# Optimization experiments

Measured on AMD Instinct MI355X. Metric: run time of the kernel, lower is better.

The kernel has to match this reference:

```python
import math
import jax, jax.numpy as jnp
import numpy as np

N_HEADS = 16

def _alibi_slopes(n_heads: int) -> np.ndarray:
    def pow2_slopes(n):
        start = 2 ** (-2 ** (-(math.log2(n) - 3)))
        return [start * start ** i for i in range(n)]
    if math.log2(n_heads).is_integer():
        slopes = pow2_slopes(n_heads)
    else:
        closest = 2 ** math.floor(math.log2(n_heads))
        slopes = pow2_slopes(closest)
        extra = pow2_slopes(2 * closest)[0::2]
        slopes = slopes + extra[: n_heads - closest]
    return np.asarray(slopes, dtype=np.float32)

def _build_alibi_bias(n_heads: int, T: int) -> jnp.ndarray:
    # (1, H, T, T): lower triangle = -slope*|i-j|, strict upper = -inf (causal)
    slopes = jnp.asarray(_alibi_slopes(n_heads))  # (H,)
    pos = jnp.arange(T)
    dist = pos[None, :] - pos[None, :].T  # (T, T), j - i
    causal = dist < 0  # future positions (j > i means dist>0? note: dist = j - i transposed)
    # match torch: distances = positions[None,:] - positions[:,None] -> dist[i,j] = j - i
    dist = pos[None, :] - pos[:, None]
    causal = dist > 0  # wait: torch masks distances < 0 where distances[i,j] = j - i? No:
    # torch: distances = positions.unsqueeze(0) - positions.unsqueeze(1) -> dist[i,j] = positions[j] - positions[i]? 
    # unsqueeze(0): (1,T) row j; unsqueeze(1): (T,1) row i -> dist[i,j] = pos[j] - pos[i]
    # causal_mask = dist < 0 masks j < i ... but then bias upper triangle kept?
    # Actually torch masks where distances < 0, i.e., j < i (past). That seems inverted,
    # but we must be FAITHFUL: mask fills -inf where pos[j] - pos[i] < 0.
    d = pos[None, :] - pos[:, None]  # d[i,j] = j - i
    mask = d < 0
    bias = -slopes[:, None, None] * jnp.abs(d).astype(jnp.float32)[None, :, :]
    bias = jnp.where(mask[None, :, :], -jnp.inf, bias)
    return bias[None]  # (1, H, T, T)

def setup_inputs() -> dict:
    key = jax.random.key(0)
    k1, k2, k3 = jax.random.split(key, 3)
    B, T, D = 2, 2048, 1024
    x = jax.random.normal(k1, (B, T, D), dtype=jnp.float32)
    W_qkv = jax.random.normal(k2, (D, 3 * D), dtype=jnp.float32) * (1.0 / math.sqrt(D))
    W_out = jax.random.normal(k3, (D, D), dtype=jnp.float32) * (1.0 / math.sqrt(D))
    return {"x": x, "W_qkv": W_qkv, "W_out": W_out}

def reference(x, W_qkv, W_out):
    B, T, D = x.shape
    H = N_HEADS
    hd = D // H
    qkv = x @ W_qkv  # (B, T, 3D)
    q, k, v = jnp.split(qkv, 3, axis=-1)
    q = q.reshape(B, T, H, hd).transpose(0, 2, 1, 3)  # (B,H,T,hd)
    k = k.reshape(B, T, H, hd).transpose(0, 2, 1, 3)
    v = v.reshape(B, T, H, hd).transpose(0, 2, 1, 3)
    scale = 1.0 / math.sqrt(hd)
    attn = jnp.einsum('bhqd,bhkd->bhqk', q, k) * scale  # (B,H,T,T)
    attn = attn + _build_alibi_bias(H, T)
    attn = jax.nn.softmax(attn, axis=-1)
    out = jnp.einsum('bhqk,bhkd->bhqd', attn, v)  # (B,H,T,hd)
    out = out.transpose(0, 2, 1, 3).reshape(B, T, D)
    return out @ W_out
```

## Files before the change

### kernel.cpp

```cpp
#include <hip/hip_runtime.h>

#define DEV __device__ __forceinline__

typedef __attribute__((ext_vector_type(4))) float f32x4;
typedef __attribute__((ext_vector_type(16))) float f32x16;
typedef __attribute__((ext_vector_type(8))) short s16x8;

static constexpr int TB  = 2;
static constexpr int TT  = 2048;
static constexpr int TD  = 1024;
static constexpr int TH  = 16;
static constexpr int THD = 64;
static constexpr int TN3 = 3072;
static constexpr int TM  = TB * TT;

#define WS_FLAG   0u
#define WS_XB     1024u
#define WS_WQKVT  (WS_XB + 8388608u)
#define WS_WOUTT  (WS_WQKVT + 6291456u)
#define WS_QKV    (WS_WOUTT + 2097152u)
#define WS_VT     (WS_QKV + 25165824u)
#define WS_CTX    (WS_VT + 8388608u)

DEV unsigned short f2bf(float f) {
  unsigned int u = __builtin_bit_cast(unsigned int, f);
  u += 0x7FFFu + ((u >> 16) & 1u);
  return (unsigned short)(u >> 16);
}
DEV f32x4 mfma16(s16x8 a, s16x8 b, f32x4 c) {
  return __builtin_amdgcn_mfma_f32_16x16x32_bf16(a, b, c, 0, 0, 0);
}
DEV f32x16 mfma32(s16x8 a, s16x8 b, f32x16 c) {
  return __builtin_amdgcn_mfma_f32_32x32x16_bf16(a, b, c, 0, 0, 0);
}
DEV void gload_lds16(const void* g, void* l) {
  __builtin_amdgcn_global_load_lds(
      (const __attribute__((address_space(1))) void*)g,
      (__attribute__((address_space(3))) void*)l, 16, 0, 0);
}
DEV unsigned int cvtpk(float lo, float hi_) {
  unsigned int r;
  asm("v_cvt_pk_bf16_f32 %0, %1, %2" : "=v"(r) : "v"(lo), "v"(hi_));
  return r;
}
DEV void plswap(unsigned int& a, unsigned int& b) {
  asm("v_permlane32_swap_b32 %0, %1" : "+v"(a), "+v"(b));
}

__global__ __launch_bounds__(256) void detect_kernel(const uint4* __restrict__ probe,
                                                     int* __restrict__ flag) {
  __shared__ int cnt;
  if (threadIdx.x == 0) cnt = 0;
  __syncthreads();
  uint4 v = probe[threadIdx.x];
  int local = 0;
  unsigned int w[4] = {v.x, v.y, v.z, v.w};
#pragma unroll
  for (int k = 0; k < 4; ++k) {
    unsigned int e0 = (w[k] >> 7) & 0xFF;
    unsigned int e1 = (w[k] >> 23) & 0xFF;
    if (e0 >= 135) local++;
    if (e1 >= 135) local++;
  }
  atomicAdd(&cnt, local);
  __syncthreads();
  if (threadIdx.x == 0) flag[0] = (cnt < 100) ? 1 : 0;
}

__global__ __launch_bounds__(256) void prep_kernel(const void* __restrict__ x,
                                                   const void* __restrict__ wqkv,
                                                   const void* __restrict__ wout,
                                                   unsigned short* __restrict__ xb,
                                                   unsigned short* __restrict__ wqkvt,
                                                   unsigned short* __restrict__ woutt,
                                                   const int* __restrict__ flag) {
  __shared__ unsigned short tile[64 * 65];
  const int bid = blockIdx.x;
  const bool bf = (flag[0] != 0);
  if (bid < 1024) {
    const void* W; unsigned short* Wt; int N, k0, n0;
    if (bid < 768) { W = wqkv; Wt = wqkvt; N = TN3; k0 = (bid & 15) * 64; n0 = (bid >> 4) * 64; }
    else { int id = bid - 768; W = wout; Wt = woutt; N = TD; k0 = (id & 15) * 64; n0 = (id >> 4) * 64; }
    for (int e = threadIdx.x; e < 4096; e += 256) {
      int kr = e >> 6, nc = e & 63;
      unsigned short v;
      if (bf) v = ((const unsigned short*)W)[(size_t)(k0 + kr) * N + n0 + nc];
      else    v = f2bf(((const float*)W)[(size_t)(k0 + kr) * N + n0 + nc]);
      tile[kr * 65 + nc] = v;
    }
    __syncthreads();
    for (int e = threadIdx.x; e < 4096; e += 256) {
      int nr = e >> 6, kc = e & 63;
      Wt[(size_t)(n0 + nr) * TD + k0 + kc] = tile[kc * 65 + nr];
    }
  } else {
    int i = (bid - 1024) * 256 + threadIdx.x;
    if (i >= (TM * TD) / 8) return;
    if (bf) {
      ((uint4*)xb)[i] = ((const uint4*)x)[i];
    } else {
      const float* s = (const float*)x + (size_t)i * 8;
      unsigned int w0 = (unsigned int)f2bf(s[0]) | ((unsigned int)f2bf(s[1]) << 16);
      unsigned int w1 = (unsigned int)f2bf(s[2]) | ((unsigned int)f2bf(s[3]) << 16);
      unsigned int w2 = (unsigned int)f2bf(s[4]) | ((unsigned int)f2bf(s[5]) << 16);
      unsigned int w3 = (unsigned int)f2bf(s[6]) | ((unsigned int)f2bf(s[7]) << 16);
      uint4 o; o.x = w0; o.y = w1; o.z = w2; o.w = w3;
      ((uint4*)xb)[i] = o;
    }
  }
}

__global__ __launch_bounds__(512, 2) void gemm_8p_kernel(const unsigned short* __restrict__ A,
                                                         const unsigned short* __restrict__ Bt,
                                                         unsigned short* __restrict__ C,
                                                         unsigned short* __restrict__ vtb,
                                                         int Mn, int Nn, int Kn) {
  __shared__ unsigned short lA[2][256 * 64];
  __shared__ unsigned short lB[2][256 * 64];
  const int tid = threadIdx.x;
  const int lane = tid & 63;
  const int wid = tid >> 6;
  const int wm = wid >> 2, wn = wid & 3;
  const int l15 = lane & 15, lg = lane >> 4;

  const int nby = Nn >> 8;
  const int nwg = (Mn >> 8) * nby;
  const int cpx = nwg >> 3;
  const int bid = blockIdx.x;
  const int swz = (bid & 7) * cpx + (bid >> 3);
  const int bm = swz / nby, bn = swz % nby;
  const int row0 = bm << 8, col0 = bn << 8;

  const int srow = tid >> 3;
  const int scol = ((tid & 7) ^ (srow & 7)) * 8;
  const unsigned short* aS = A  + (size_t)(row0 + srow) * Kn + scol;
  const unsigned short* bS = Bt + (size_t)(col0 + srow) * Kn + scol;
  const size_t r64 = (size_t)64 * Kn;

#define STG(dst, src, koff, h) do {                                        \
    unsigned short* _d = (dst) + (h) * 8192 + tid * 8;                     \
    const unsigned short* _s = (src) + (size_t)(h) * 2 * r64 + (koff);     \
    gload_lds16(_s, _d);                                                   \
    gload_lds16(_s + r64, _d + 4096);                                      \
  } while (0)

  f32x4 acc[8][4];
#pragma unroll
  for (int m = 0; m < 8; ++m)
#pragma unroll
    for (int n = 0; n < 4; ++n) acc[m][n] = (f32x4){0.f, 0.f, 0.f, 0.f};

  const int sa = l15 & 7;
  const int kc0 = (lg ^ sa) * 8;
  const int kc1 = ((4 + lg) ^ sa) * 8;
  const int aRow = (wm * 128 + l15) * 64;
  const int bRow = (wn * 64 + l15) * 64;

  STG(&lA[0][0], aS, 0, 0); STG(&lA[0][0], aS, 0, 1);
  STG(&lB[0][0], bS, 0, 0); STG(&lB[0][0], bS, 0, 1);
  asm volatile("s_waitcnt vmcnt(0)" ::: "memory");
  __builtin_amdgcn_s_barrier();

  const int nt = Kn >> 6;
  for (int t = 0; t < nt; ++t) {
    const unsigned short* la = &lA[t & 1][0];
    const unsigned short* lb = &lB[t & 1][0];
    unsigned short* na = &lA[(t + 1) & 1][0];
    unsigned short* nb = &lB[(t + 1) & 1][0];
    const int koff = (t + 1) << 6;
    const bool more = (t + 1 < nt);

    s16x8 af[4][2], b0[2][2], b1[2][2];

#pragma unroll
    for (int m = 0; m < 4; ++m) {
      af[m][0] = *(const s16x8*)&la[aRow + m * 1024 + kc0];
      af[m][1] = *(const s16x8*)&la[aRow + m * 1024 + kc1];
    }
#pragma unroll
    for (int n = 0; n < 2; ++n) {
      b0[n][0] = *(const s16x8*)&lb[bRow + n * 1024 + kc0];
      b0[n][1] = *(const s16x8*)&lb[bRow + n * 1024 + kc1];
    }
    if (more) STG(na, aS, koff, 0);
    __builtin_amdgcn_s_barrier();
    asm volatile("s_waitcnt lgkmcnt(0)" ::: "memory");
    __builtin_amdgcn_sched_barrier(0);
    __builtin_amdgcn_s_setprio(1);
#pragma unroll
    for (int m = 0; m < 4; ++m)
#pragma unroll
      for (int n = 0; n < 2; ++n) {
        acc[m][n] = mfma16(af[m][0], b0[n][0], acc[m][n]);
        acc[m][n] = mfma16(af[m][1], b0[n][1], acc[m][n]);
      }
    __builtin_amdgcn_s_setprio(0);
    if (more) asm volatile("s_waitcnt vmcnt(4)" ::: "memory");
    else      asm volatile("s_waitcnt vmcnt(1)" ::: "memory");
    __builtin_amdgcn_s_barrier();

#pragma unroll
    for (int n = 0; n < 2; ++n) {
      b1[n][0] = *(const s16x8*)&lb[bRow + (2 + n) * 1024 + kc0];
      b1[n][1] = *(const s16x8*)&lb[bRow + (2 + n) * 1024 + kc1];
    }
    if (more) STG(nb, bS, koff, 0);
    __builtin_amdgcn_s_barrier();
    asm volatile("s_waitcnt lgkmcnt(0)" ::: "memory");
    __builtin_amdgcn_sched_barrier(0);
    __builtin_amdgcn_s_setprio(1);
#pragma unroll
    for (int m = 0; m < 4; ++m)
#pragma unroll
      for (int n = 0; n < 2; ++n) {
        acc[m][2 + n] = mfma16(af[m][0], b1[n][0], acc[m][2 + n]);
        acc[m][2 + n] = mfma16(af[m][1], b1[n][1], acc[m][2 + n]);
      }
    __builtin_amdgcn_s_setprio(0);
    if (more) asm volatile("s_waitcnt vmcnt(4)" ::: "memory");
    else      asm volatile("s_waitcnt vmcnt(0)" ::: "memory");
    __builtin_amdgcn_s_barrier();

#pragma unroll
    for (int m = 0; m < 4; ++m) {
      af[m][0] = *(const s16x8*)&la[aRow + (4 + m) * 1024 + kc0];
      af[m][1] = *(const s16x8*)&la[aRow + (4 + m) * 1024 + kc1];
    }
    if (more) STG(nb, bS, koff, 1);
    __builtin_amdgcn_s_barrier();
    asm volatile("s_waitcnt lgkmcnt(0)" ::: "memory");
    __builtin_amdgcn_sched_barrier(0);
    __builtin_amdgcn_s_setprio(1);
#pragma unroll
    for (int m = 0; m < 4; ++m)
#pragma unroll
      for (int n = 0; n < 2; ++n) {
        acc[4 + m][n] = mfma16(af[m][0], b0[n][0], acc[4 + m][n]);
        acc[4 + m][n] = mfma16(af[m][1], b0[n][1], acc[4 + m][n]);
      }
    __builtin_amdgcn_s_setprio(0);
    __builtin_amdgcn_s_barrier();

    if (more) STG(na, aS, koff, 1);
    __builtin_amdgcn_s_barrier();
    __builtin_amdgcn_sched_barrier(0);
    __builtin_amdgcn_s_setprio(1);
#pragma unroll
    for (int m = 0; m < 4; ++m)
#pragma unroll
      for (int n = 0; n < 2; ++n) {
        acc[4 + m][2 + n] = mfma16(af[m][0], b1[n][0], acc[4 + m][2 + n]);
        acc[4 + m][2 + n] = mfma16(af[m][1], b1[n][1], acc[4 + m][2 + n]);
      }
    __builtin_amdgcn_s_setprio(0);
    if (more) asm volatile("s_waitcnt vmcnt(4)" ::: "memory");
    __builtin_amdgcn_s_barrier();
  }
#undef STG

  if (col0 < 2048) {
    unsigned short* cw = C + (size_t)(row0 + wm * 128 + lg * 4) * Nn + col0 + wn * 64 + l15;
#pragma unroll
    for (int m = 0; m < 8; ++m)
#pragma unroll
      for (int n = 0; n < 4; ++n)
#pragma unroll
        for (int j = 0; j < 4; ++j)
          cw[(size_t)(m * 16 + j) * Nn + n * 16] = f2bf(acc[m][n][j]);
  } else {
    const int cb0 = col0 + wn * 64 + l15 - 2048;
    const int t0r = row0 + wm * 128 + lg * 4;
#pragma unroll
    for (int m = 0; m < 8; ++m) {
      int tg = t0r + m * 16;
      int bb = tg >> 11, tt = tg & 2047;
#pragma unroll
      for (int n = 0; n < 4; ++n) {
        int cc2 = cb0 + n * 16;
        int h = cc2 >> 6, d = cc2 & 63;
        unsigned short* dst = vtb + (((size_t)(bb * 16 + h) * 64 + d) << 11) + tt;
        uint2 pk;
        pk.x = cvtpk(acc[m][n][0], acc[m][n][1]);
        pk.y = cvtpk(acc[m][n][2], acc[m][n][3]);
        *(uint2*)dst = pk;
      }
    }
  }
}

__global__ __launch_bounds__(256) void gemm_bt2_kernel(const unsigned short* __restrict__ A,
                                                       const unsigned short* __restrict__ Bt,
                                                       void* __restrict__ Cout,
                                                       int Mn, int Nn, int Kn,
                                                       const int* __restrict__ flag) {
  __shared__ unsigned short lA[2][128 * 32];
  __shared__ unsigned short lB[2][64 * 32];
  const int tid  = threadIdx.x;
  const int lane = tid & 63, wid = tid >> 6;
  const int wr = wid >> 1, wc = wid & 1;
  const int l15 = lane & 15, lg = lane >> 4;
  const int row0 = blockIdx.x * 128, col0 = blockIdx.y * 64;

  f32x4 acc[4][2];
#pragma unroll
  for (int m = 0; m < 4; ++m)
#pragma unroll
    for (int n = 0; n < 2; ++n) acc[m][n] = (f32x4){0.f, 0.f, 0.f, 0.f};

  const int srow = tid >> 2;
  const int scol = ((tid & 3) ^ (srow & 3)) * 8;
  const unsigned short* aS = A  + (size_t)(row0 + srow) * Kn + scol;
  const unsigned short* bS = Bt + (size_t)(col0 + srow) * Kn + scol;
  const size_t r64 = (size_t)64 * Kn;

#define STG2(bi) do {                                        \
    unsigned short* _da = &lA[bi][0] + tid * 8;              \
    gload_lds16(aS,       _da);                              \
    gload_lds16(aS + r64, _da + 2048);                       \
    if (srow < 64) gload_lds16(bS, &lB[bi][0] + tid * 8);    \
  } while (0)

  const int rd = (lg ^ (l15 & 3)) * 8;
  const int aoff = (wr * 64 + l15) * 32 + rd;
  const int boff = (wc * 32 + l15) * 32 + rd;

  STG2(0); aS += 32; bS += 32;
  __syncthreads();

  const int nt = Kn >> 5;
  for (int t = 0; t < nt; ++t) {
    if (t + 1 < nt) { STG2((t + 1) & 1); aS += 32; bS += 32; }
    const unsigned short* la = &lA[t & 1][0];
    const unsigned short* lb = &lB[t & 1][0];
    s16x8 af[4], bfv[2];
#pragma unroll
    for (int m = 0; m < 4; ++m) af[m] = *(const s16x8*)&la[aoff + m * 512];
#pragma unroll
    for (int n = 0; n < 2; ++n) bfv[n] = *(const s16x8*)&lb[boff + n * 512];
    __builtin_amdgcn_s_setprio(1);
#pragma unroll
    for (int m = 0; m < 4; ++m)
#pragma unroll
      for (int n = 0; n < 2; ++n)
        acc[m][n] = mfma16(af[m], bfv[n], acc[m][n]);
    __builtin_amdgcn_s_setprio(0);
    __syncthreads();
  }
#undef STG2

  const bool obf = (flag[0] != 0);
#pragma unroll
  for (int m = 0; m < 4; ++m)
#pragma unroll
    for (int n = 0; n < 2; ++n)
#pragma unroll
      for (int j = 0; j < 4; ++j) {
        int r = row0 + wr * 64 + m * 16 + lg * 4 + j;
        int c = col0 + wc * 32 + n * 16 + l15;
        if (obf) ((unsigned short*)Cout)[(size_t)r * Nn + c] = f2bf(acc[m][n][j]);
        else     ((float*)Cout)[(size_t)r * Nn + c] = acc[m][n][j];
      }
}

__global__ __launch_bounds__(256, 4) void attn_kernel(const unsigned short* __restrict__ qkv,
                                                      const unsigned short* __restrict__ vt,
                                                      unsigned short* __restrict__ ctx) {
  __shared__ __align__(16) unsigned char smem[32768];
  unsigned short* kl0 = (unsigned short*)smem;
  unsigned short* vl0 = (unsigned short*)(smem + 16384);
  float* red = (float*)smem;

  const int bid = blockIdx.x;
  const int r_ = bid & 255, q_ = bid >> 8;
  const int s_ = r_ >> 5, g_ = r_ & 31;
  const int bh = (g_ + 8 * q_) & 31;
  const int x32 = (q_ == 0) ? s_ : (q_ == 1) ? 15 - s_ : (q_ == 2) ? 16 + s_ : 31 - s_;
  const int b = bh >> 4, h = bh & 15;

  const int tid = threadIdx.x;
  const int wid = tid >> 6, lane = tid & 63;
  const int wr = wid & 1, wk = wid >> 1;
  const int l31 = lane & 31, hi = lane >> 5;
  const int i_base = x32 * 64 + wr * 32;

  const unsigned short* qb  = qkv + (size_t)b * TT * TN3 + h * THD;
  const unsigned short* kb_ = qkv + (size_t)b * TT * TN3 + TD + h * THD;
  const unsigned short* vb_ = vt + (size_t)bh * THD * TT;

  const float LOG2E = 1.44269504f;
  const float SL2 = exp2f(-0.5f * (float)(h + 1)) * LOG2E;
  const float SC2 = 0.125f * LOG2E;
  const float dbias = -SL2 * 64.0f;

  const int t_rel = (int)((140.0f / SL2 + 63.0f) * (1.0f / 64.0f)) + 1;
  const int t_end = (32 < x32 + t_rel) ? 32 : x32 + t_rel;

  const int srow = tid >> 3;
  const int sx = ((tid & 7) ^ (srow & 7)) * 8;
  const unsigned short* srcK = kb_ + (size_t)(x32 * 64 + srow) * TN3 + sx;
  const unsigned short* srcV = vb_ + (size_t)srow * TT + x32 * 64 + sx;
  const size_t kstep = (size_t)64 * TN3;

#define STAGE(bufi) do {                                   \
    unsigned short* _dk = kl0 + (bufi) * 4096 + tid * 8;   \
    unsigned short* _dv = vl0 + (bufi) * 4096 + tid * 8;   \
    gload_lds16(srcK,            _dk);                     \
    gload_lds16(srcK + 32 * TN3, _dk + 2048);              \
    gload_lds16(srcV,            _dv);                     \
    gload_lds16(srcV + 32 * TT,  _dv + 2048);              \
  } while (0)

  s16x8 qa[4];
  {
    const unsigned short* qr = qb + (size_t)(i_base + l31) * TN3 + hi * 8;
#pragma unroll
    for (int dd = 0; dd < 4; ++dd) qa[dd] = *(const s16x8*)(qr + dd * 16);
  }

  s16x8 ones;
  {
    short ov = (l31 == 0) ? (short)0x3F80 : (short)0;
#pragma unroll
    for (int e = 0; e < 8; ++e) ones[e] = ov;
  }

  float base[16];
#pragma unroll
  for (int r = 0; r < 16; ++r) {
    int cr0 = (r & 3) + 8 * (r >> 2);
    base[r] = -SL2 * (float)(wk * 32 + cr0 + 4 * hi - wr * 32 - l31) - 16.0f;
  }

  f32x16 o0, o1, ol;
#pragma unroll
  for (int r = 0; r < 16; ++r) { o0[r] = 0.f; o1[r] = 0.f; ol[r] = 0.f; }

  const int sw = (l31 & 7) << 4;
  int cc[4];
#pragma unroll
  for (int dd = 0; dd < 4; ++dd) cc[dd] = ((dd * 32 + hi * 16) ^ sw) >> 1;

  int cur = 0;
  STAGE(0); srcK += kstep; srcV += 64;
  asm volatile("s_waitcnt vmcnt(0)" ::: "memory");
  __syncthreads();

  for (int t = x32; t < t_end; ++t) {
    if (t + 1 < t_end) { STAGE(cur ^ 1); srcK += kstep; srcV += 64; }

    const unsigned short* kb = kl0 + cur * 4096;
    const unsigned short* vbl = vl0 + cur * 4096;

    f32x16 sv;
#pragma unroll
    for (int r = 0; r < 16; ++r) sv[r] = 0.f;
    __builtin_amdgcn_s_setprio(1);
#pragma unroll
    for (int dd = 0; dd < 4; ++dd) {
      s16x8 k0 = *(const s16x8*)&kb[(wk * 32 + l31) * 64 + cc[dd]];
      sv = mfma32(k0, qa[dd], sv);
    }
    __builtin_amdgcn_s_setprio(0);

    if (t == x32) {
#pragma unroll
      for (int r = 0; r < 16; ++r) {
        float bb = base[r];
        float v = __builtin_amdgcn_exp2f(fmaf(sv[r], SC2, bb));
        sv[r] = (bb > -15.999f) ? 0.0f : v;
      }
    } else {
#pragma unroll
      for (int r = 0; r < 16; ++r)
        sv[r] = __builtin_amdgcn_exp2f(fmaf(sv[r], SC2, base[r]));
    }
#pragma unroll
    for (int r = 0; r < 16; ++r) base[r] += dbias;

    s16x8 pa[2];
#pragma unroll
    for (int mh = 0; mh < 2; ++mh) {
      unsigned int a0 = cvtpk(sv[8 * mh + 0], sv[8 * mh + 1]);
      unsigned int a1 = cvtpk(sv[8 * mh + 2], sv[8 * mh + 3]);
      unsigned int b0 = cvtpk(sv[8 * mh + 4], sv[8 * mh + 5]);
      unsigned int b1 = cvtpk(sv[8 * mh + 6], sv[8 * mh + 7]);
      plswap(a0, b0); plswap(a1, b1);
      uint4 u; u.x = a0; u.y = a1; u.z = b0; u.w = b1;
      pa[mh] = __builtin_bit_cast(s16x8, u);
    }

    __builtin_amdgcn_s_setprio(1);
#pragma unroll
    for (int ks = 0; ks < 2; ++ks) {
      s16x8 v0 = *(const s16x8*)&vbl[l31 * 64 + cc[wk * 2 + ks]];
      s16x8 v1 = *(const s16x8*)&vbl[(32 + l31) * 64 + cc[wk * 2 + ks]];
      o0 = mfma32(pa[ks], v0, o0);
      o1 = mfma32(pa[ks], v1, o1);
      ol = mfma32(pa[ks], ones, ol);
    }
    __builtin_amdgcn_s_setprio(0);

    asm volatile("s_waitcnt vmcnt(0)" ::: "memory");
    __syncthreads();
    cur ^= 1;
  }
#undef STAGE

  const int rbase = (wr * 64 + lane) * 49;
  if (wk == 1) {
#pragma unroll
    for (int r = 0; r < 16; ++r) red[rbase + r] = o0[r];
#pragma unroll
    for (int r = 0; r < 16; ++r) red[rbase + 16 + r] = o1[r];
#pragma unroll
    for (int r = 0; r < 16; ++r) red[rbase + 32 + r] = ol[r];
  }
  __syncthreads();
  if (wk == 0) {
#pragma unroll
    for (int r = 0; r < 16; ++r) o0[r] += red[rbase + r];
#pragma unroll
    for (int r = 0; r < 16; ++r) o1[r] += red[rbase + 16 + r];
#pragma unroll
    for (int r = 0; r < 16; ++r) ol[r] += red[rbase + 32 + r];

    float rdiv[16];
#pragma unroll
    for (int r = 0; r < 16; ++r) rdiv[r] = 1.0f / __shfl(ol[r], lane & 32);

    unsigned short* cb = ctx + (size_t)(b * TT + i_base) * TD + h * THD + l31;
#pragma unroll
    for (int r = 0; r < 16; ++r) {
      int row = (r & 3) + 8 * (r >> 2) + 4 * hi;
      unsigned int pk = cvtpk(o0[r] * rdiv[r], o1[r] * rdiv[r]);
      cb[(size_t)row * TD] = (unsigned short)pk;
      cb[(size_t)row * TD + 32] = (unsigned short)(pk >> 16);
    }
  }
}

extern "C" void kernel_launch(void* const* d_in, const int* in_sizes, int n_in,
                              void* d_out, int out_size, void* d_ws, size_t ws_size,
                              hipStream_t stream) {
  const void* x    = d_in[0];
  const void* wqkv = d_in[1];
  const void* wout = d_in[2];
  char* ws = (char*)d_ws;
  int* flag             = (int*)(ws + WS_FLAG);
  unsigned short* xb    = (unsigned short*)(ws + WS_XB);
  unsigned short* wqkvt = (unsigned short*)(ws + WS_WQKVT);
  unsigned short* woutt = (unsigned short*)(ws + WS_WOUTT);
  unsigned short* qkvb  = (unsigned short*)(ws + WS_QKV);
  unsigned short* vtb   = (unsigned short*)(ws + WS_VT);
  unsigned short* ctxb  = (unsigned short*)(ws + WS_CTX);

  detect_kernel<<<1, 256, 0, stream>>>((const uint4*)x, flag);
  prep_kernel<<<3072, 256, 0, stream>>>(x, wqkv, wout, xb, wqkvt, woutt, flag);
  gemm_8p_kernel<<<(TM / 256) * (TN3 / 256), 512, 0, stream>>>(xb, wqkvt, qkvb, vtb, TM, TN3, TD);
  attn_kernel<<<1024, 256, 0, stream>>>(qkvb, vtb, ctxb);
  gemm_bt2_kernel<<<dim3(TM / 128, TD / 64), 256, 0, stream>>>(ctxb, woutt, d_out, TM, TD, TD, flag);
}
```

Baseline: 113.0 us.

## Restructure QKV GEMM k-phases and triple-buffer the output-projection GEMM

The main QKV GEMM inner loop is reorganized: instead of splitting along M and N halves, it loads all eight A fragments per k-half and iterates over k-halves, issuing the next tile's global-to-LDS loads in two larger batches and waiting on vmcnt(0) at the end. The output-projection GEMM moves from a double-buffered K=32 tile to a triple-buffered K=64 tile that prefetches two steps ahead, with swizzled LDS reads and raw barriers replacing __syncthreads. The intent is to hide global latency better and cut barrier count per K. In exchange it raises LDS use, caps occupancy via launch bounds, and holds more A-fragment registers in the first kernel.

```diff
diff --git a/kernel.cpp b/kernel.cpp
--- a/kernel.cpp
+++ b/kernel.cpp
@@ -170,90 +170,69 @@
     const int koff = (t + 1) << 6;
     const bool more = (t + 1 < nt);
 
-    s16x8 af[4][2], b0[2][2], b1[2][2];
-
-#pragma unroll
-    for (int m = 0; m < 4; ++m) {
-      af[m][0] = *(const s16x8*)&la[aRow + m * 1024 + kc0];
-      af[m][1] = *(const s16x8*)&la[aRow + m * 1024 + kc1];
-    }
-#pragma unroll
-    for (int n = 0; n < 2; ++n) {
-      b0[n][0] = *(const s16x8*)&lb[bRow + n * 1024 + kc0];
-      b0[n][1] = *(const s16x8*)&lb[bRow + n * 1024 + kc1];
-    }
-    if (more) STG(na, aS, koff, 0);
+    s16x8 af[8], bv[2];
+
+#pragma unroll
+    for (int m = 0; m < 8; ++m) af[m] = *(const s16x8*)&la[aRow + m * 1024 + kc0];
+    bv[0] = *(const s16x8*)&lb[bRow + kc0];
+    bv[1] = *(const s16x8*)&lb[bRow + 1024 + kc0];
+    if (more) { STG(na, aS, koff, 0); STG(na, aS, koff, 1); }
     __builtin_amdgcn_s_barrier();
     asm volatile("s_waitcnt lgkmcnt(0)" ::: "memory");
     __builtin_amdgcn_sched_barrier(0);
     __builtin_amdgcn_s_setprio(1);
 #pragma unroll
-    for (int m = 0; m < 4; ++m)
-#pragma unroll
-      for (int n = 0; n < 2; ++n) {
-        acc[m][n] = mfma16(af[m][0], b0[n][0], acc[m][n]);
-        acc[m][n] = mfma16(af[m][1], b0[n][1], acc[m][n]);
-      }
-    __builtin_amdgcn_s_setprio(0);
-    if (more) asm volatile("s_waitcnt vmcnt(4)" ::: "memory");
-    else      asm volatile("s_waitcnt vmcnt(1)" ::: "memory");
-    __builtin_amdgcn_s_barrier();
-
-#pragma unroll
-    for (int n = 0; n < 2; ++n) {
-      b1[n][0] = *(const s16x8*)&lb[bRow + (2 + n) * 1024 + kc0];
-      b1[n][1] = *(const s16x8*)&lb[bRow + (2 + n) * 1024 + kc1];
-    }
-    if (more) STG(nb, bS, koff, 0);
+    for (int m = 0; m < 8; ++m) {
+      acc[m][0] = mfma16(af[m], bv[0], acc[m][0]);
+      acc[m][1] = mfma16(af[m], bv[1], acc[m][1]);
+    }
+    __builtin_amdgcn_s_setprio(0);
+    __builtin_amdgcn_s_barrier();
+
+    bv[0] = *(const s16x8*)&lb[bRow + 2048 + kc0];
+    bv[1] = *(const s16x8*)&lb[bRow + 3072 + kc0];
+    if (more) { STG(nb, bS, koff, 0); STG(nb, bS, koff, 1); }
     __builtin_amdgcn_s_barrier();
     asm volatile("s_waitcnt lgkmcnt(0)" ::: "memory");
     __builtin_amdgcn_sched_barrier(0);
     __builtin_amdgcn_s_setprio(1);
 #pragma unroll
-    for (int m = 0; m < 4; ++m)
-#pragma unroll
-      for (int n = 0; n < 2; ++n) {
-        acc[m][2 + n] = mfma16(af[m][0], b1[n][0], acc[m][2 + n]);
-        acc[m][2 + n] = mfma16(af[m][1], b1[n][1], acc[m][2 + n]);
-      }
-    __builtin_amdgcn_s_setprio(0);
-    if (more) asm volatile("s_waitcnt vmcnt(4)" ::: "memory");
-    else      asm volatile("s_waitcnt vmcnt(0)" ::: "memory");
-    __builtin_amdgcn_s_barrier();
-
-#pragma unroll
-    for (int m = 0; m < 4; ++m) {
-      af[m][0] = *(const s16x8*)&la[aRow + (4 + m) * 1024 + kc0];
-      af[m][1] = *(const s16x8*)&la[aRow + (4 + m) * 1024 + kc1];
-    }
-    if (more) STG(nb, bS, koff, 1);
+    for (int m = 0; m < 8; ++m) {
+      acc[m][2] = mfma16(af[m], bv[0], acc[m][2]);
+      acc[m][3] = mfma16(af[m], bv[1], acc[m][3]);
+    }
+    __builtin_amdgcn_s_setprio(0);
+    __builtin_amdgcn_s_barrier();
+
+#pragma unroll
+    for (int m = 0; m < 8; ++m) af[m] = *(const s16x8*)&la[aRow + m * 1024 + kc1];
+    bv[0] = *(const s16x8*)&lb[bRow + kc1];
+    bv[1] = *(const s16x8*)&lb[bRow + 1024 + kc1];
     __builtin_amdgcn_s_barrier();
     asm volatile("s_waitcnt lgkmcnt(0)" ::: "memory");
     __builtin_amdgcn_sched_barrier(0);
     __builtin_amdgcn_s_setprio(1);
 #pragma unroll
-    for (int m = 0; m < 4; ++m)
-#pragma unroll
-      for (int n = 0; n < 2; ++n) {
-        acc[4 + m][n] = mfma16(af[m][0], b0[n][0], acc[4 + m][n]);
-        acc[4 + m][n] = mfma16(af[m][1], b0[n][1], acc[4 + m][n]);
-      }
-    __builtin_amdgcn_s_setprio(0);
-    __builtin_amdgcn_s_barrier();
-
-    if (more) STG(na, aS, koff, 1);
-    __builtin_amdgcn_s_barrier();
+    for (int m = 0; m < 8; ++m) {
+      acc[m][0] = mfma16(af[m], bv[0], acc[m][0]);
+      acc[m][1] = mfma16(af[m], bv[1], acc[m][1]);
+    }
+    __builtin_amdgcn_s_setprio(0);
+    __builtin_amdgcn_s_barrier();
+
+    bv[0] = *(const s16x8*)&lb[bRow + 2048 + kc1];
+    bv[1] = *(const s16x8*)&lb[bRow + 3072 + kc1];
+    __builtin_amdgcn_s_barrier();
+    asm volatile("s_waitcnt lgkmcnt(0)" ::: "memory");
     __builtin_amdgcn_sched_barrier(0);
     __builtin_amdgcn_s_setprio(1);
 #pragma unroll
-    for (int m = 0; m < 4; ++m)
-#pragma unroll
-      for (int n = 0; n < 2; ++n) {
-        acc[4 + m][2 + n] = mfma16(af[m][0], b1[n][0], acc[4 + m][2 + n]);
-        acc[4 + m][2 + n] = mfma16(af[m][1], b1[n][1], acc[4 + m][2 + n]);
-      }
-    __builtin_amdgcn_s_setprio(0);
-    if (more) asm volatile("s_waitcnt vmcnt(4)" ::: "memory");
+    for (int m = 0; m < 8; ++m) {
+      acc[m][2] = mfma16(af[m], bv[0], acc[m][2]);
+      acc[m][3] = mfma16(af[m], bv[1], acc[m][3]);
+    }
+    __builtin_amdgcn_s_setprio(0);
+    asm volatile("s_waitcnt vmcnt(0)" ::: "memory");
     __builtin_amdgcn_s_barrier();
   }
 #undef STG
@@ -288,13 +267,13 @@
   }
 }
 
-__global__ __launch_bounds__(256) void gemm_bt2_kernel(const unsigned short* __restrict__ A,
-                                                       const unsigned short* __restrict__ Bt,
-                                                       void* __restrict__ Cout,
-                                                       int Mn, int Nn, int Kn,
-                                                       const int* __restrict__ flag) {
-  __shared__ unsigned short lA[2][128 * 32];
-  __shared__ unsigned short lB[2][64 * 32];
+__global__ __launch_bounds__(256, 2) void gemm_bt2_kernel(const unsigned short* __restrict__ A,
+                                                          const unsigned short* __restrict__ Bt,
+                                                          void* __restrict__ Cout,
+                                                          int Mn, int Nn, int Kn,
+                                                          const int* __restrict__ flag) {
+  __shared__ unsigned short lA[3][128 * 64];
+  __shared__ unsigned short lB[3][64 * 64];
   const int tid  = threadIdx.x;
   const int lane = tid & 63, wid = tid >> 6;
   const int wr = wid >> 1, wc = wid & 1;
@@ -307,36 +286,50 @@
 #pragma unroll
     for (int n = 0; n < 2; ++n) acc[m][n] = (f32x4){0.f, 0.f, 0.f, 0.f};
 
-  const int srow = tid >> 2;
-  const int scol = ((tid & 3) ^ (srow & 3)) * 8;
+  const int srow = tid >> 3;
+  const int scol = ((tid & 7) ^ (srow & 7)) * 8;
   const unsigned short* aS = A  + (size_t)(row0 + srow) * Kn + scol;
   const unsigned short* bS = Bt + (size_t)(col0 + srow) * Kn + scol;
-  const size_t r64 = (size_t)64 * Kn;
-
-#define STG2(bi) do {                                        \
-    unsigned short* _da = &lA[bi][0] + tid * 8;              \
-    gload_lds16(aS,       _da);                              \
-    gload_lds16(aS + r64, _da + 2048);                       \
-    if (srow < 64) gload_lds16(bS, &lB[bi][0] + tid * 8);    \
+  const size_t r32 = (size_t)32 * Kn;
+
+#define STG2(bi, koff) do {                                                 \
+    unsigned short* _da = &lA[bi][0] + tid * 8;                             \
+    unsigned short* _db = &lB[bi][0] + tid * 8;                             \
+    gload_lds16(aS + (koff),            _da);                               \
+    gload_lds16(aS + (koff) + r32,      _da + 2048);                        \
+    gload_lds16(aS + (koff) + 2 * r32,  _da + 4096);                        \
+    gload_lds16(aS + (koff) + 3 * r32,  _da + 6144);                        \
+    gload_lds16(bS + (koff),            _db);                               \
+    gload_lds16(bS + (koff) + r32,      _db + 2048);                        \
   } while (0)
 
-  const int rd = (lg ^ (l15 & 3)) * 8;
-  const int aoff = (wr * 64 + l15) * 32 + rd;
-  const int boff = (wc * 32 + l15) * 32 + rd;
-
-  STG2(0); aS += 32; bS += 32;
-  __syncthreads();
-
-  const int nt = Kn >> 5;
+  const int sa = l15 & 7;
+  const int kc0 = (lg ^ sa) * 8;
+  const int kc1 = ((4 + lg) ^ sa) * 8;
+  const int aoff = (wr * 64 + l15) * 64;
+  const int boff = (wc * 32 + l15) * 64;
+
+  const int nt = Kn >> 6;
+  STG2(0, 0);
+  STG2(1, 64);
+  asm volatile("s_waitcnt vmcnt(6)" ::: "memory");
+  __builtin_amdgcn_s_barrier();
+
+  int cur = 0;
   for (int t = 0; t < nt; ++t) {
-    if (t + 1 < nt) { STG2((t + 1) & 1); aS += 32; bS += 32; }
-    const unsigned short* la = &lA[t & 1][0];
-    const unsigned short* lb = &lB[t & 1][0];
+    const unsigned short* la = &lA[cur][0];
+    const unsigned short* lb = &lB[cur][0];
+    const bool deep = (t + 2 < nt);
+
     s16x8 af[4], bfv[2];
 #pragma unroll
-    for (int m = 0; m < 4; ++m) af[m] = *(const s16x8*)&la[aoff + m * 512];
-#pragma unroll
-    for (int n = 0; n < 2; ++n) bfv[n] = *(const s16x8*)&lb[boff + n * 512];
+    for (int m = 0; m < 4; ++m) af[m] = *(const s16x8*)&la[aoff + m * 1024 + kc0];
+#pragma unroll
+    for (int n = 0; n < 2; ++n) bfv[n] = *(const s16x8*)&lb[boff + n * 1024 + kc0];
+    if (deep) { int nbuf = (cur + 2 == 3) ? 0 : ((cur + 2 == 4) ? 1 : cur + 2); STG2(nbuf, (t + 2) << 6); }
+    __builtin_amdgcn_s_barrier();
+    asm volatile("s_waitcnt lgkmcnt(0)" ::: "memory");
+    __builtin_amdgcn_sched_barrier(0);
     __builtin_amdgcn_s_setprio(1);
 #pragma unroll
     for (int m = 0; m < 4; ++m)
@@ -344,7 +337,28 @@
       for (int n = 0; n < 2; ++n)
         acc[m][n] = mfma16(af[m], bfv[n], acc[m][n]);
     __builtin_amdgcn_s_setprio(0);
-    __syncthreads();
+    __builtin_amdgcn_s_barrier();
+
+#pragma unroll
+    for (int m = 0; m < 4; ++m) af[m] = *(const s16x8*)&la[aoff + m * 1024 + kc1];
+#pragma unroll
+    for (int n = 0; n < 2; ++n) bfv[n] = *(const s16x8*)&lb[boff + n * 1024 + kc1];
+    __builtin_amdgcn_s_barrier();
+    asm volatile("s_waitcnt lgkmcnt(0)" ::: "memory");
+    __builtin_amdgcn_sched_barrier(0);
+    __builtin_amdgcn_s_setprio(1);
+#pragma unroll
+    for (int m = 0; m < 4; ++m)
+#pragma unroll
+      for (int n = 0; n < 2; ++n)
+        acc[m][n] = mfma16(af[m], bfv[n], acc[m][n]);
+    __builtin_amdgcn_s_setprio(0);
+    if (t + 1 < nt) {
+      if (deep) asm volatile("s_waitcnt vmcnt(6)" ::: "memory");
+      else      asm volatile("s_waitcnt vmcnt(0)" ::: "memory");
+      __builtin_amdgcn_s_barrier();
+    }
+    cur = (cur == 2) ? 0 : cur + 1;
   }
 #undef STG2
 
```

Measured after the change: 110.1 us. 2.5% less time.
